# Kernel optimization log

Hardware: AMD Instinct MI355X
Metric: run time of the kernel (lower is better)

Reference implementation:

```python
import jax, jax.numpy as jnp
import numpy as np

T, E, H, I, K = 2048, 16, 2048, 1408, 4
NORM_TOPK_PROB = True
W_SCALE = 0.02  # realistic init scale to keep activations sane


def setup_inputs() -> dict:
    key = jax.random.key(0)
    k_x, k_r, k_g, k_u, k_d = jax.random.split(key, 5)
    return {
        "x": jax.random.normal(k_x, (T, H), jnp.float32),
        "router_logits": jax.random.normal(k_r, (T, E), jnp.float32),
        "gate_w": jax.random.normal(k_g, (E, I, H), jnp.float32) * W_SCALE,
        "up_w": jax.random.normal(k_u, (E, I, H), jnp.float32) * W_SCALE,
        "down_w": jax.random.normal(k_d, (E, H, I), jnp.float32) * W_SCALE,
    }


def reference(x, router_logits, gate_w, up_w, down_w):
    # Router: softmax over experts, take top-k, optionally renormalize.
    probs = jax.nn.softmax(router_logits.astype(jnp.float32), axis=-1)  # [T, E]
    top_vals, top_idx = jax.lax.top_k(probs, K)                          # [T, K]
    if NORM_TOPK_PROB:
        top_vals = top_vals / jnp.sum(top_vals, axis=-1, keepdims=True)
    # Dense combine weights [T, E]: zero for unselected experts.
    combine = jnp.einsum("tke,tk->te", jax.nn.one_hot(top_idx, E, dtype=top_vals.dtype), top_vals)
    combine = combine.astype(x.dtype)

    # GLU per expert: down( silu(gate(x)) * up(x) ), combined by routing weights.
    g = jnp.einsum("th,eih->tei", x, gate_w)   # [T, E, I]
    u = jnp.einsum("th,eih->tei", x, up_w)     # [T, E, I]
    h = jax.nn.silu(g) * u                      # [T, E, I]
    out = jnp.einsum("tei,ehi,te->th", h, down_w, combine)  # [T, H]
    return out
```

## Files before the change

kernel.cpp:

```cpp
#include <hip/hip_runtime.h>
#include <hip/hip_bf16.h>
#include <math.h>

#define TTOK 2048
#define NEXP 16
#define HDIM 2048
#define IDIM 1408
#define TOPK 4

typedef __attribute__((ext_vector_type(8))) short short8;
typedef __attribute__((ext_vector_type(4))) float floatx4;

#define GUP ((size_t)NEXP * IDIM * HDIM)

#define LDSP(p) ((__attribute__((address_space(3))) void*)(p))
#define GLBP(p) ((const __attribute__((address_space(1))) void*)(p))

__device__ __forceinline__ unsigned short f2bf(float f) {
    unsigned u = __builtin_bit_cast(unsigned, f);
    u += 0x7FFFu + ((u >> 16) & 1u);
    return (unsigned short)(u >> 16);
}

__device__ __forceinline__ void cvt8(const float* __restrict__ s, unsigned short* __restrict__ d) {
    const float4* sv = (const float4*)s;
    float4 a = sv[0], b = sv[1];
    union { unsigned short h[8]; uint4 v; } p;
    p.h[0] = f2bf(a.x); p.h[1] = f2bf(a.y); p.h[2] = f2bf(a.z); p.h[3] = f2bf(a.w);
    p.h[4] = f2bf(b.x); p.h[5] = f2bf(b.y); p.h[6] = f2bf(b.z); p.h[7] = f2bf(b.w);
    *(uint4*)d = p.v;
}

__global__ void zero_f32(float* __restrict__ p, size_t n) {
    size_t i = (size_t)blockIdx.x * blockDim.x + threadIdx.x;
    size_t stride = (size_t)gridDim.x * blockDim.x;
    for (; i < n; i += stride) p[i] = 0.f;
}

__global__ void zero_i32(int* __restrict__ p, int n) {
    int i = threadIdx.x;
    if (i < n) p[i] = 0;
}

__global__ void cast_weights(const float* __restrict__ g, const float* __restrict__ u,
                             const float* __restrict__ d,
                             unsigned short* __restrict__ og, unsigned short* __restrict__ ou,
                             unsigned short* __restrict__ od) {
    size_t i = ((size_t)blockIdx.x * blockDim.x + threadIdx.x) * 8;
    size_t stride = (size_t)gridDim.x * blockDim.x * 8;
    for (; i < GUP; i += stride) {
        cvt8(g + i, og + i);
        cvt8(u + i, ou + i);
        cvt8(d + i, od + i);
    }
}

__global__ void router_kernel(const float* __restrict__ logits,
                              int* __restrict__ cnt,
                              int* __restrict__ tok_id,
                              float* __restrict__ tok_w) {
    int t = blockIdx.x * blockDim.x + threadIdx.x;
    if (t >= TTOK) return;
    float l[NEXP];
#pragma unroll
    for (int e = 0; e < NEXP; ++e) l[e] = logits[t * NEXP + e];
    int bi[TOPK]; float bv[TOPK];
    unsigned used = 0;
#pragma unroll
    for (int k = 0; k < TOPK; ++k) {
        float best = -1e30f; int b = 0;
#pragma unroll
        for (int e = 0; e < NEXP; ++e) {
            if (!((used >> e) & 1u) && l[e] > best) { best = l[e]; b = e; }
        }
        used |= 1u << b; bi[k] = b; bv[k] = best;
    }
    float m = bv[0], w[TOPK], s = 0.f;
#pragma unroll
    for (int k = 0; k < TOPK; ++k) { w[k] = expf(bv[k] - m); s += w[k]; }
    float inv = 1.f / s;
#pragma unroll
    for (int k = 0; k < TOPK; ++k) {
        int e = bi[k];
        int pos = atomicAdd(&cnt[e], 1);
        tok_id[e * TTOK + pos] = t;
        tok_w[e * TTOK + pos] = w[k] * inv;
    }
}

__global__ void scan_kernel(const int* __restrict__ cnt, int* __restrict__ offs) {
    if (threadIdx.x == 0 && blockIdx.x == 0) {
        int a = 0;
        for (int e = 0; e < NEXP; ++e) {
            offs[e] = a;
            a += (cnt[e] + 127) & ~127;
        }
        offs[NEXP] = a;
    }
}

__global__ void gather_x(const float* __restrict__ x, const int* __restrict__ cnt,
                         const int* __restrict__ offs, const int* __restrict__ tok_id,
                         unsigned short* __restrict__ xg) {
    int e = blockIdx.y, slot = blockIdx.x;
    int n = cnt[e];
    int padcap = (n + 127) & ~127;
    if (slot >= padcap) return;
    unsigned short* dst = xg + (size_t)(offs[e] + slot) * HDIM;
    int tid = threadIdx.x;
    if (slot < n) {
        const float* src = x + (size_t)tok_id[e * TTOK + slot] * HDIM;
        cvt8(src + tid * 8, dst + tid * 8);
    } else {
        uint4 z = {0u, 0u, 0u, 0u};
        ((uint4*)dst)[tid] = z;
    }
}

__launch_bounds__(256)
__global__ void gateup_mfma(const unsigned short* __restrict__ xg,
                            const unsigned short* __restrict__ gw,
                            const unsigned short* __restrict__ uw,
                            const int* __restrict__ cnt, const int* __restrict__ offs,
                            const float* __restrict__ tok_w,
                            unsigned short* __restrict__ hbuf) {
    const int e = blockIdx.z;
    const int n = cnt[e];
    const int m0 = blockIdx.y * 128;
    if (m0 >= n) return;
    const int i0 = blockIdx.x * 128;
    const int rowbase = offs[e];

    __shared__ __align__(16) unsigned short sA[128 * 64];
    __shared__ __align__(16) unsigned short sBg[128 * 64];
    __shared__ __align__(16) unsigned short sBu[128 * 64];

    const int tid = threadIdx.x;
    const int lane = tid & 63;
    const int wave = tid >> 6;
    const int wm = wave >> 1;
    const int wn = wave & 1;

    const unsigned short* Abase = xg + (size_t)(rowbase + m0) * HDIM;
    const unsigned short* Gbase = gw + (size_t)e * IDIM * HDIM + (size_t)i0 * HDIM;
    const unsigned short* Ubase = uw + (size_t)e * IDIM * HDIM + (size_t)i0 * HDIM;

    floatx4 accg[4][4], accu[4][4];
#pragma unroll
    for (int i = 0; i < 4; ++i)
#pragma unroll
        for (int j = 0; j < 4; ++j) {
            accg[i][j] = (floatx4){0.f, 0.f, 0.f, 0.f};
            accu[i][j] = (floatx4){0.f, 0.f, 0.f, 0.f};
        }

    const int lrow = lane >> 3;
    const int lcol = (lane & 7) * 8;

    for (int k0 = 0; k0 < HDIM; k0 += 64) {
        for (int c = wave; c < 48; c += 4) {
            int t = c >> 4;
            int ch = c & 15;
            int r = ch * 8 + lrow;
            const unsigned short* gsrc =
                (t == 0) ? Abase + (size_t)r * HDIM + k0 + lcol
              : (t == 1) ? Gbase + (size_t)r * HDIM + k0 + lcol
                         : Ubase + (size_t)r * HDIM + k0 + lcol;
            unsigned short* lds = ((t == 0) ? sA : (t == 1) ? sBg : sBu) + ch * 512 + lane * 8;
            __builtin_amdgcn_global_load_lds(GLBP(gsrc), LDSP(lds), 16, 0, 0);
        }
        __syncthreads();
#pragma unroll
        for (int s = 0; s < 2; ++s) {
            short8 af[4], bg[4], bu[4];
            const int ko = s * 32 + (lane >> 4) * 8;
            const int mrow = wm * 64 + (lane & 15);
            const int nrow = wn * 64 + (lane & 15);
#pragma unroll
            for (int i = 0; i < 4; ++i)
                af[i] = *(const short8*)&sA[(mrow + i * 16) * 64 + ko];
#pragma unroll
            for (int j = 0; j < 4; ++j) {
                bg[j] = *(const short8*)&sBg[(nrow + j * 16) * 64 + ko];
                bu[j] = *(const short8*)&sBu[(nrow + j * 16) * 64 + ko];
            }
#pragma unroll
            for (int i = 0; i < 4; ++i)
#pragma unroll
                for (int j = 0; j < 4; ++j) {
                    accg[i][j] = __builtin_amdgcn_mfma_f32_16x16x32_bf16(af[i], bg[j], accg[i][j], 0, 0, 0);
                    accu[i][j] = __builtin_amdgcn_mfma_f32_16x16x32_bf16(af[i], bu[j], accu[i][j], 0, 0, 0);
                }
        }
        __syncthreads();
    }

    const int q = lane >> 4;
    const int cl = lane & 15;
#pragma unroll
    for (int i = 0; i < 4; ++i) {
#pragma unroll
        for (int r = 0; r < 4; ++r) {
            int slot = m0 + wm * 64 + i * 16 + q * 4 + r;
            if (slot < n) {
                float wgt = tok_w[e * TTOK + slot];
                size_t rowoff = (size_t)(rowbase + slot) * IDIM + i0 + wn * 64 + cl;
#pragma unroll
                for (int j = 0; j < 4; ++j) {
                    float g = accg[i][j][r];
                    float u = accu[i][j][r];
                    float h = (g / (1.f + __expf(-g))) * u * wgt;
                    hbuf[rowoff + j * 16] = f2bf(h);
                }
            }
        }
    }
}

__launch_bounds__(256)
__global__ void down_mfma(const unsigned short* __restrict__ hbuf,
                          const unsigned short* __restrict__ dw,
                          const int* __restrict__ cnt, const int* __restrict__ offs,
                          const int* __restrict__ tok_id,
                          float* __restrict__ out) {
    const int e = blockIdx.z;
    const int n = cnt[e];
    const int m0 = blockIdx.y * 128;
    if (m0 >= n) return;
    const int h0 = blockIdx.x * 128;
    const int rowbase = offs[e];

    __shared__ __align__(16) unsigned short sA[128 * 64];
    __shared__ __align__(16) unsigned short sB[128 * 64];

    const int tid = threadIdx.x;
    const int lane = tid & 63;
    const int wave = tid >> 6;
    const int wm = wave >> 1;
    const int wn = wave & 1;

    const unsigned short* Abase = hbuf + (size_t)(rowbase + m0) * IDIM;
    const unsigned short* Bbase = dw + (size_t)e * HDIM * IDIM + (size_t)h0 * IDIM;

    floatx4 acc[4][4];
#pragma unroll
    for (int i = 0; i < 4; ++i)
#pragma unroll
        for (int j = 0; j < 4; ++j) acc[i][j] = (floatx4){0.f, 0.f, 0.f, 0.f};

    const int lrow = lane >> 3;
    const int lcol = (lane & 7) * 8;

    for (int k0 = 0; k0 < IDIM; k0 += 64) {
        for (int c = wave; c < 32; c += 4) {
            int t = c >> 4;
            int ch = c & 15;
            int r = ch * 8 + lrow;
            const unsigned short* gsrc =
                (t == 0) ? Abase + (size_t)r * IDIM + k0 + lcol
                         : Bbase + (size_t)r * IDIM + k0 + lcol;
            unsigned short* lds = ((t == 0) ? sA : sB) + ch * 512 + lane * 8;
            __builtin_amdgcn_global_load_lds(GLBP(gsrc), LDSP(lds), 16, 0, 0);
        }
        __syncthreads();
#pragma unroll
        for (int s = 0; s < 2; ++s) {
            short8 af[4], bf[4];
            const int ko = s * 32 + (lane >> 4) * 8;
            const int mrow = wm * 64 + (lane & 15);
            const int nrow = wn * 64 + (lane & 15);
#pragma unroll
            for (int i = 0; i < 4; ++i)
                af[i] = *(const short8*)&sA[(mrow + i * 16) * 64 + ko];
#pragma unroll
            for (int j = 0; j < 4; ++j)
                bf[j] = *(const short8*)&sB[(nrow + j * 16) * 64 + ko];
#pragma unroll
            for (int i = 0; i < 4; ++i)
#pragma unroll
                for (int j = 0; j < 4; ++j)
                    acc[i][j] = __builtin_amdgcn_mfma_f32_16x16x32_bf16(af[i], bf[j], acc[i][j], 0, 0, 0);
        }
        __syncthreads();
    }

    const int q = lane >> 4;
    const int cl = lane & 15;
#pragma unroll
    for (int i = 0; i < 4; ++i) {
#pragma unroll
        for (int r = 0; r < 4; ++r) {
            int slot = m0 + wm * 64 + i * 16 + q * 4 + r;
            if (slot < n) {
                int t = tok_id[e * TTOK + slot];
                float* orow = out + (size_t)t * HDIM + h0 + wn * 64 + cl;
#pragma unroll
                for (int j = 0; j < 4; ++j) atomicAdd(&orow[j * 16], acc[i][j][r]);
            }
        }
    }
}

extern "C" void kernel_launch(void* const* d_in, const int* in_sizes, int n_in,
                              void* d_out, int out_size, void* d_ws, size_t ws_size,
                              hipStream_t stream) {
    const float* x      = (const float*)d_in[0];
    const float* logits = (const float*)d_in[1];
    const float* gate_w = (const float*)d_in[2];
    const float* up_w   = (const float*)d_in[3];
    const float* down_w = (const float*)d_in[4];
    float* out = (float*)d_out;

    char* ws = (char*)d_ws;
    int*   cnt    = (int*)(ws);
    int*   offs   = (int*)(ws + 64);
    int*   tok_id = (int*)(ws + 1024);
    float* tok_w  = (float*)(ws + 1024 + TTOK * NEXP * 4);
    unsigned short* gate_bf = (unsigned short*)(ws + (1u << 20));
    unsigned short* up_bf   = gate_bf + GUP;
    unsigned short* down_bf = up_bf + GUP;
    unsigned short* xg   = (unsigned short*)(ws + (size_t)280 * (1u << 20));
    unsigned short* hbuf = (unsigned short*)(ws + (size_t)321 * (1u << 20));

    zero_i32<<<1, 32, 0, stream>>>(cnt, NEXP);
    zero_f32<<<1024, 256, 0, stream>>>(out, (size_t)TTOK * HDIM);
    cast_weights<<<4096, 256, 0, stream>>>(gate_w, up_w, down_w, gate_bf, up_bf, down_bf);
    router_kernel<<<TTOK / 256, 256, 0, stream>>>(logits, cnt, tok_id, tok_w);
    scan_kernel<<<1, 1, 0, stream>>>(cnt, offs);
    {
        dim3 g(TTOK, NEXP);
        gather_x<<<g, 256, 0, stream>>>(x, cnt, offs, tok_id, xg);
    }
    {
        dim3 g(IDIM / 128, TTOK / 128, NEXP);
        gateup_mfma<<<g, 256, 0, stream>>>(xg, gate_bf, up_bf, cnt, offs, tok_w, hbuf);
    }
    {
        dim3 g(HDIM / 128, TTOK / 128, NEXP);
        down_mfma<<<g, 256, 0, stream>>>(hbuf, down_bf, cnt, offs, tok_id, out);
    }
}
```

Before: 1.073 ms.

## Double-buffer GEMM K-tiles and replace scatter atomics with partial-buffer reduction

Both expert GEMMs now use two LDS buffers with 32-wide K tiles. The next tile is fetched into the spare buffer while MFMAs run on the current one, leaving a single barrier per iteration. The down-projection no longer does float atomicAdd into the output. It writes per-slot partial rows into a scratch buffer that reuses the no-longer-needed gate weight region, and a new reduce kernel sums each token's top-k rows using a token-to-(expert,pos) map recorded by the router. This drops the output zeroing pass and the atomic contention, at the cost of an extra fp32 partial buffer write and read, plus twice as many K iterations.

```diff
diff --git a/kernel.cpp b/kernel.cpp
--- a/kernel.cpp
+++ b/kernel.cpp
@@ -1,5 +1,4 @@
 #include <hip/hip_runtime.h>
-#include <hip/hip_bf16.h>
 #include <math.h>
 
 #define TTOK 2048
@@ -29,12 +28,6 @@
     p.h[0] = f2bf(a.x); p.h[1] = f2bf(a.y); p.h[2] = f2bf(a.z); p.h[3] = f2bf(a.w);
     p.h[4] = f2bf(b.x); p.h[5] = f2bf(b.y); p.h[6] = f2bf(b.z); p.h[7] = f2bf(b.w);
     *(uint4*)d = p.v;
-}
-
-__global__ void zero_f32(float* __restrict__ p, size_t n) {
-    size_t i = (size_t)blockIdx.x * blockDim.x + threadIdx.x;
-    size_t stride = (size_t)gridDim.x * blockDim.x;
-    for (; i < n; i += stride) p[i] = 0.f;
 }
 
 __global__ void zero_i32(int* __restrict__ p, int n) {
@@ -58,7 +51,8 @@
 __global__ void router_kernel(const float* __restrict__ logits,
                               int* __restrict__ cnt,
                               int* __restrict__ tok_id,
-                              float* __restrict__ tok_w) {
+                              float* __restrict__ tok_w,
+                              int* __restrict__ tk_ep) {
     int t = blockIdx.x * blockDim.x + threadIdx.x;
     if (t >= TTOK) return;
     float l[NEXP];
@@ -85,6 +79,7 @@
         int pos = atomicAdd(&cnt[e], 1);
         tok_id[e * TTOK + pos] = t;
         tok_w[e * TTOK + pos] = w[k] * inv;
+        tk_ep[t * TOPK + k] = (e << 16) | pos;
     }
 }
 
@@ -131,9 +126,9 @@
     const int i0 = blockIdx.x * 128;
     const int rowbase = offs[e];
 
-    __shared__ __align__(16) unsigned short sA[128 * 64];
-    __shared__ __align__(16) unsigned short sBg[128 * 64];
-    __shared__ __align__(16) unsigned short sBu[128 * 64];
+    __shared__ __align__(16) unsigned short sA[2][128 * 32];
+    __shared__ __align__(16) unsigned short sBg[2][128 * 32];
+    __shared__ __align__(16) unsigned short sBu[2][128 * 32];
 
     const int tid = threadIdx.x;
     const int lane = tid & 63;
@@ -154,54 +149,61 @@
             accu[i][j] = (floatx4){0.f, 0.f, 0.f, 0.f};
         }
 
-    const int lrow = lane >> 3;
-    const int lcol = (lane & 7) * 8;
-
-    for (int k0 = 0; k0 < HDIM; k0 += 64) {
-        for (int c = wave; c < 48; c += 4) {
-            int t = c >> 4;
-            int ch = c & 15;
-            int r = ch * 8 + lrow;
-            const unsigned short* gsrc =
-                (t == 0) ? Abase + (size_t)r * HDIM + k0 + lcol
-              : (t == 1) ? Gbase + (size_t)r * HDIM + k0 + lcol
-                         : Ubase + (size_t)r * HDIM + k0 + lcol;
-            unsigned short* lds = ((t == 0) ? sA : (t == 1) ? sBg : sBu) + ch * 512 + lane * 8;
-            __builtin_amdgcn_global_load_lds(GLBP(gsrc), LDSP(lds), 16, 0, 0);
-        }
+    const int srow = lane >> 2;
+    const int scol = (lane & 3) * 8;
+
+    auto stage = [&](int buf, int k0) {
+#pragma unroll
+        for (int q = 0; q < 2; ++q) {
+            const int ch = q * 4 + wave;
+            const int r = ch * 16 + srow;
+            const size_t go = (size_t)r * HDIM + k0 + scol;
+            const int lo = ch * 512 + lane * 8;
+            __builtin_amdgcn_global_load_lds(GLBP(Abase + go), LDSP(&sA[buf][lo]), 16, 0, 0);
+            __builtin_amdgcn_global_load_lds(GLBP(Gbase + go), LDSP(&sBg[buf][lo]), 16, 0, 0);
+            __builtin_amdgcn_global_load_lds(GLBP(Ubase + go), LDSP(&sBu[buf][lo]), 16, 0, 0);
+        }
+    };
+
+    stage(0, 0);
+    __syncthreads();
+
+    const int ko = (lane >> 4) * 8;
+    const int mrow = wm * 64 + (lane & 15);
+    const int nrow = wn * 64 + (lane & 15);
+
+    int cur = 0;
+    for (int k0 = 0; k0 < HDIM; k0 += 32) {
+        const int nb = cur ^ 1;
+        if (k0 + 32 < HDIM) stage(nb, k0 + 32);
+
+        short8 af[4], bg[4], bu[4];
+#pragma unroll
+        for (int i = 0; i < 4; ++i)
+            af[i] = *(const short8*)&sA[cur][(mrow + i * 16) * 32 + ko];
+#pragma unroll
+        for (int j = 0; j < 4; ++j) {
+            bg[j] = *(const short8*)&sBg[cur][(nrow + j * 16) * 32 + ko];
+            bu[j] = *(const short8*)&sBu[cur][(nrow + j * 16) * 32 + ko];
+        }
+#pragma unroll
+        for (int i = 0; i < 4; ++i)
+#pragma unroll
+            for (int j = 0; j < 4; ++j) {
+                accg[i][j] = __builtin_amdgcn_mfma_f32_16x16x32_bf16(af[i], bg[j], accg[i][j], 0, 0, 0);
+                accu[i][j] = __builtin_amdgcn_mfma_f32_16x16x32_bf16(af[i], bu[j], accu[i][j], 0, 0, 0);
+            }
         __syncthreads();
-#pragma unroll
-        for (int s = 0; s < 2; ++s) {
-            short8 af[4], bg[4], bu[4];
-            const int ko = s * 32 + (lane >> 4) * 8;
-            const int mrow = wm * 64 + (lane & 15);
-            const int nrow = wn * 64 + (lane & 15);
-#pragma unroll
-            for (int i = 0; i < 4; ++i)
-                af[i] = *(const short8*)&sA[(mrow + i * 16) * 64 + ko];
-#pragma unroll
-            for (int j = 0; j < 4; ++j) {
-                bg[j] = *(const short8*)&sBg[(nrow + j * 16) * 64 + ko];
-                bu[j] = *(const short8*)&sBu[(nrow + j * 16) * 64 + ko];
-            }
-#pragma unroll
-            for (int i = 0; i < 4; ++i)
-#pragma unroll
-                for (int j = 0; j < 4; ++j) {
-                    accg[i][j] = __builtin_amdgcn_mfma_f32_16x16x32_bf16(af[i], bg[j], accg[i][j], 0, 0, 0);
-                    accu[i][j] = __builtin_amdgcn_mfma_f32_16x16x32_bf16(af[i], bu[j], accu[i][j], 0, 0, 0);
-                }
-        }
-        __syncthreads();
-    }
-
-    const int q = lane >> 4;
+        cur = nb;
+    }
+
+    const int qe = lane >> 4;
     const int cl = lane & 15;
 #pragma unroll
     for (int i = 0; i < 4; ++i) {
 #pragma unroll
         for (int r = 0; r < 4; ++r) {
-            int slot = m0 + wm * 64 + i * 16 + q * 4 + r;
+            int slot = m0 + wm * 64 + i * 16 + qe * 4 + r;
             if (slot < n) {
                 float wgt = tok_w[e * TTOK + slot];
                 size_t rowoff = (size_t)(rowbase + slot) * IDIM + i0 + wn * 64 + cl;
@@ -221,8 +223,7 @@
 __global__ void down_mfma(const unsigned short* __restrict__ hbuf,
                           const unsigned short* __restrict__ dw,
                           const int* __restrict__ cnt, const int* __restrict__ offs,
-                          const int* __restrict__ tok_id,
-                          float* __restrict__ out) {
+                          float* __restrict__ pbuf) {
     const int e = blockIdx.z;
     const int n = cnt[e];
     const int m0 = blockIdx.y * 128;
@@ -230,8 +231,8 @@
     const int h0 = blockIdx.x * 128;
     const int rowbase = offs[e];
 
-    __shared__ __align__(16) unsigned short sA[128 * 64];
-    __shared__ __align__(16) unsigned short sB[128 * 64];
+    __shared__ __align__(16) unsigned short sA[2][128 * 32];
+    __shared__ __align__(16) unsigned short sB[2][128 * 32];
 
     const int tid = threadIdx.x;
     const int lane = tid & 63;
@@ -248,57 +249,81 @@
 #pragma unroll
         for (int j = 0; j < 4; ++j) acc[i][j] = (floatx4){0.f, 0.f, 0.f, 0.f};
 
-    const int lrow = lane >> 3;
-    const int lcol = (lane & 7) * 8;
-
-    for (int k0 = 0; k0 < IDIM; k0 += 64) {
-        for (int c = wave; c < 32; c += 4) {
-            int t = c >> 4;
-            int ch = c & 15;
-            int r = ch * 8 + lrow;
-            const unsigned short* gsrc =
-                (t == 0) ? Abase + (size_t)r * IDIM + k0 + lcol
-                         : Bbase + (size_t)r * IDIM + k0 + lcol;
-            unsigned short* lds = ((t == 0) ? sA : sB) + ch * 512 + lane * 8;
-            __builtin_amdgcn_global_load_lds(GLBP(gsrc), LDSP(lds), 16, 0, 0);
-        }
+    const int srow = lane >> 2;
+    const int scol = (lane & 3) * 8;
+
+    auto stage = [&](int buf, int k0) {
+#pragma unroll
+        for (int q = 0; q < 2; ++q) {
+            const int ch = q * 4 + wave;
+            const int r = ch * 16 + srow;
+            const size_t go = (size_t)r * IDIM + k0 + scol;
+            const int lo = ch * 512 + lane * 8;
+            __builtin_amdgcn_global_load_lds(GLBP(Abase + go), LDSP(&sA[buf][lo]), 16, 0, 0);
+            __builtin_amdgcn_global_load_lds(GLBP(Bbase + go), LDSP(&sB[buf][lo]), 16, 0, 0);
+        }
+    };
+
+    stage(0, 0);
+    __syncthreads();
+
+    const int ko = (lane >> 4) * 8;
+    const int mrow = wm * 64 + (lane & 15);
+    const int nrow = wn * 64 + (lane & 15);
+
+    int cur = 0;
+    for (int k0 = 0; k0 < IDIM; k0 += 32) {
+        const int nb = cur ^ 1;
+        if (k0 + 32 < IDIM) stage(nb, k0 + 32);
+
+        short8 af[4], bf[4];
+#pragma unroll
+        for (int i = 0; i < 4; ++i)
+            af[i] = *(const short8*)&sA[cur][(mrow + i * 16) * 32 + ko];
+#pragma unroll
+        for (int j = 0; j < 4; ++j)
+            bf[j] = *(const short8*)&sB[cur][(nrow + j * 16) * 32 + ko];
+#pragma unroll
+        for (int i = 0; i < 4; ++i)
+#pragma unroll
+            for (int j = 0; j < 4; ++j)
+                acc[i][j] = __builtin_amdgcn_mfma_f32_16x16x32_bf16(af[i], bf[j], acc[i][j], 0, 0, 0);
         __syncthreads();
-#pragma unroll
-        for (int s = 0; s < 2; ++s) {
-            short8 af[4], bf[4];
-            const int ko = s * 32 + (lane >> 4) * 8;
-            const int mrow = wm * 64 + (lane & 15);
-            const int nrow = wn * 64 + (lane & 15);
-#pragma unroll
-            for (int i = 0; i < 4; ++i)
-                af[i] = *(const short8*)&sA[(mrow + i * 16) * 64 + ko];
-#pragma unroll
-            for (int j = 0; j < 4; ++j)
-                bf[j] = *(const short8*)&sB[(nrow + j * 16) * 64 + ko];
-#pragma unroll
-            for (int i = 0; i < 4; ++i)
-#pragma unroll
-                for (int j = 0; j < 4; ++j)
-                    acc[i][j] = __builtin_amdgcn_mfma_f32_16x16x32_bf16(af[i], bf[j], acc[i][j], 0, 0, 0);
-        }
-        __syncthreads();
-    }
-
-    const int q = lane >> 4;
+        cur = nb;
+    }
+
+    const int qe = lane >> 4;
     const int cl = lane & 15;
 #pragma unroll
     for (int i = 0; i < 4; ++i) {
 #pragma unroll
         for (int r = 0; r < 4; ++r) {
-            int slot = m0 + wm * 64 + i * 16 + q * 4 + r;
+            int slot = m0 + wm * 64 + i * 16 + qe * 4 + r;
             if (slot < n) {
-                int t = tok_id[e * TTOK + slot];
-                float* orow = out + (size_t)t * HDIM + h0 + wn * 64 + cl;
-#pragma unroll
-                for (int j = 0; j < 4; ++j) atomicAdd(&orow[j * 16], acc[i][j][r]);
+                float* orow = pbuf + (size_t)(rowbase + slot) * HDIM + h0 + wn * 64 + cl;
+#pragma unroll
+                for (int j = 0; j < 4; ++j) orow[j * 16] = acc[i][j][r];
             }
         }
     }
+}
+
+__global__ void reduce_out(const float* __restrict__ pbuf, const int* __restrict__ offs,
+                           const int* __restrict__ tk_ep, float* __restrict__ out) {
+    const int t = blockIdx.x;
+    const int tid = threadIdx.x;
+    float4 a0 = {0.f, 0.f, 0.f, 0.f}, a1 = {0.f, 0.f, 0.f, 0.f};
+#pragma unroll
+    for (int k = 0; k < TOPK; ++k) {
+        int v = tk_ep[t * TOPK + k];
+        int e = v >> 16, pos = v & 0xffff;
+        const float4* src = (const float4*)(pbuf + (size_t)(offs[e] + pos) * HDIM + tid * 8);
+        float4 b0 = src[0], b1 = src[1];
+        a0.x += b0.x; a0.y += b0.y; a0.z += b0.z; a0.w += b0.w;
+        a1.x += b1.x; a1.y += b1.y; a1.z += b1.z; a1.w += b1.w;
+    }
+    float4* dst = (float4*)(out + (size_t)t * HDIM + tid * 8);
+    dst[0] = a0; dst[1] = a1;
 }
 
 extern "C" void kernel_launch(void* const* d_in, const int* in_sizes, int n_in,
@@ -316,16 +341,17 @@
     int*   offs   = (int*)(ws + 64);
     int*   tok_id = (int*)(ws + 1024);
     float* tok_w  = (float*)(ws + 1024 + TTOK * NEXP * 4);
+    int*   tk_ep  = (int*)(ws + 1024 + 2 * TTOK * NEXP * 4);
     unsigned short* gate_bf = (unsigned short*)(ws + (1u << 20));
     unsigned short* up_bf   = gate_bf + GUP;
     unsigned short* down_bf = up_bf + GUP;
+    float* pbuf = (float*)(ws + (1u << 20));
     unsigned short* xg   = (unsigned short*)(ws + (size_t)280 * (1u << 20));
     unsigned short* hbuf = (unsigned short*)(ws + (size_t)321 * (1u << 20));
 
     zero_i32<<<1, 32, 0, stream>>>(cnt, NEXP);
-    zero_f32<<<1024, 256, 0, stream>>>(out, (size_t)TTOK * HDIM);
     cast_weights<<<4096, 256, 0, stream>>>(gate_w, up_w, down_w, gate_bf, up_bf, down_bf);
-    router_kernel<<<TTOK / 256, 256, 0, stream>>>(logits, cnt, tok_id, tok_w);
+    router_kernel<<<TTOK / 256, 256, 0, stream>>>(logits, cnt, tok_id, tok_w, tk_ep);
     scan_kernel<<<1, 1, 0, stream>>>(cnt, offs);
     {
         dim3 g(TTOK, NEXP);
@@ -337,6 +363,7 @@
     }
     {
         dim3 g(HDIM / 128, TTOK / 128, NEXP);
-        down_mfma<<<g, 256, 0, stream>>>(hbuf, down_bf, cnt, offs, tok_id, out);
-    }
-}
+        down_mfma<<<g, 256, 0, stream>>>(hbuf, down_bf, cnt, offs, pbuf);
+    }
+    reduce_out<<<TTOK, 256, 0, stream>>>(pbuf, offs, tk_ep, out);
+}
```

Measured after the change: 978.1 us. 8.8% less time.
